# Kernel tuning notes

Measured on AMD Instinct MI355X. Metric: run time of the kernel, lower is better.

## Reference

```python
import jax, jax.numpy as jnp
import numpy as np

D_MODEL = 1024
N_HEAD = 16
D_FF = 4096
SEQ = 2048
BATCH = 4
EPS = 1e-5


def setup_inputs() -> dict:
    key = jax.random.key(0)
    ks = jax.random.split(key, 10)
    s = 0.02
    return {
        "src": jax.random.normal(ks[0], (SEQ, BATCH, D_MODEL), jnp.float32),
        "padding_mask": jnp.zeros((BATCH, SEQ), jnp.bool_),
        "w_qkv": jax.random.normal(ks[1], (3 * D_MODEL, D_MODEL), jnp.float32) * s,
        "fc_w": jax.random.normal(ks[2], (D_MODEL, D_MODEL), jnp.float32) * s,
        "fc_b": jnp.zeros((D_MODEL,), jnp.float32),
        "w1": jax.random.normal(ks[3], (D_FF, D_MODEL), jnp.float32) * s,
        "b1": jnp.zeros((D_FF,), jnp.float32),
        "w2": jax.random.normal(ks[4], (D_MODEL, D_FF), jnp.float32) * s,
        "b2": jnp.zeros((D_MODEL,), jnp.float32),
        "g1": jnp.ones((D_MODEL,), jnp.float32),
        "be1": jnp.zeros((D_MODEL,), jnp.float32),
        "g2": jnp.ones((D_MODEL,), jnp.float32),
        "be2": jnp.zeros((D_MODEL,), jnp.float32),
    }


def _layer_norm(x, g, b):
    mu = jnp.mean(x, axis=-1, keepdims=True)
    var = jnp.mean(jnp.square(x - mu), axis=-1, keepdims=True)
    return (x - mu) * jax.lax.rsqrt(var + EPS) * g + b


def _mha(src, padding_mask, w_qkv, fc_w, fc_b):
    L, B, D = src.shape
    H = N_HEAD
    dh = D // H
    qkv = jnp.einsum("lbd,ed->lbe", src, w_qkv)  # (L,B,3D)
    q, k, v = jnp.split(qkv, 3, axis=-1)
    # (L, B*H, dh) -> (B*H, L, dh)
    q = q.reshape(L, B * H, dh).transpose(1, 0, 2)
    k = k.reshape(L, B * H, dh).transpose(1, 0, 2)
    v = v.reshape(L, B * H, dh).transpose(1, 0, 2)
    scores = jnp.einsum("nqd,nkd->nqk", q, k) / np.sqrt(dh).astype(np.float32)
    scores = scores.reshape(B, H, L, L)
    scores = jnp.where(padding_mask[:, None, None, :], -jnp.inf, scores)
    attn = jax.nn.softmax(scores, axis=-1).reshape(B * H, L, L)
    out = jnp.einsum("nqk,nkd->nqd", attn, v)  # (B*H, L, dh)
    out = out.transpose(1, 0, 2).reshape(L, B, D)
    return out @ fc_w.T + fc_b


def reference(src, padding_mask, w_qkv, fc_w, fc_b, w1, b1, w2, b2, g1, be1, g2, be2):
    src2 = _mha(src, padding_mask, w_qkv, fc_w, fc_b)
    src = _layer_norm(src + src2, g1, be1)
    h = jax.nn.relu(src @ w1.T + b1)
    src2 = h @ w2.T + b2
    return _layer_norm(src + src2, g2, be2)
```

## Files before the change

### kernel.cpp

```cpp
#include <hip/hip_runtime.h>
#include <cstdint>
#include <cstddef>

typedef __attribute__((ext_vector_type(8))) short bf16x8;
typedef __attribute__((ext_vector_type(4))) float f32x4;
typedef __attribute__((ext_vector_type(16))) float f32x16;

static __device__ __forceinline__ unsigned short f2bf(float f) {
    union { float f; unsigned u; } v; v.f = f;
    unsigned r = v.u + 0x7FFFu + ((v.u >> 16) & 1u);
    return (unsigned short)(r >> 16);
}
static __device__ __forceinline__ float bf2f(unsigned short u) {
    union { unsigned u; float f; } v; v.u = ((unsigned)u) << 16; return v.f;
}

static __device__ __forceinline__ void gld_lds16(const void* g, void* l) {
    unsigned loff = (unsigned)(size_t)l;
    loff = (unsigned)__builtin_amdgcn_readfirstlane((int)loff);
    __builtin_amdgcn_global_load_lds(
        (const __attribute__((address_space(1))) unsigned int*)(size_t)g,
        (__attribute__((address_space(3))) unsigned int*)(size_t)loff,
        16, 0, 0);
}

__global__ __launch_bounds__(256) void k_cvt5(
    const float* __restrict__ p0, const float* __restrict__ p1,
    const float* __restrict__ p2, const float* __restrict__ p3,
    const float* __restrict__ p4,
    unsigned short* __restrict__ q0, unsigned short* __restrict__ q1,
    unsigned short* __restrict__ q2, unsigned short* __restrict__ q3,
    unsigned short* __restrict__ q4)
{
    const int blk = blockIdx.x;
    const float* in; unsigned short* out; int base;
    if      (blk < 3072)  { in = p0; out = q0; base = blk; }
    else if (blk < 4096)  { in = p1; out = q1; base = blk - 3072; }
    else if (blk < 8192)  { in = p2; out = q2; base = blk - 4096; }
    else if (blk < 12288) { in = p3; out = q3; base = blk - 8192; }
    else                  { in = p4; out = q4; base = blk - 12288; }
    const int i = (base * 256 + threadIdx.x) * 4;
    float4 v = *reinterpret_cast<const float4*>(in + i);
    ushort4 o;
    o.x = f2bf(v.x); o.y = f2bf(v.y); o.z = f2bf(v.z); o.w = f2bf(v.w);
    *reinterpret_cast<ushort4*>(out + i) = o;
}

template<int BM, int MF>
__global__ __launch_bounds__(512, 2) void k_gemm8(
    const unsigned short* __restrict__ A, const unsigned short* __restrict__ W,
    float* __restrict__ Cf, unsigned short* __restrict__ Cb,
    const float* __restrict__ bias,
    int M, int N, int K, int scale_cols, float scale, int relu)
{
    __shared__ unsigned short As[2][BM * 64];
    __shared__ unsigned short Bs[2][256 * 64];
    const int tid = threadIdx.x, wid = tid >> 6, lane = tid & 63;
    const int lr = lane & 15, g16 = (lane >> 4) * 16;
    const int wm = wid >> 2, wn = wid & 3;

    const int nbx = N >> 8;
    const int nwg = gridDim.x;
    const int raw = blockIdx.x;
    const int swz = (raw & 7) * (nwg >> 3) + (raw >> 3);
    const int bm = (swz / nbx) * BM, bn = (swz % nbx) * 256;

    const int rin = tid >> 3;
    const int cole = (((tid & 7) * 16) ^ ((rin & 7) << 4)) >> 1;

    auto STAGE = [&](int bb, int kt1) {
        #pragma unroll
        for (int c = 0; c < BM / 64; ++c)
            gld_lds16(A + (size_t)(bm + c * 64 + rin) * K + kt1 + cole,
                      (char*)As[bb] + c * 8192 + wid * 1024);
        #pragma unroll
        for (int c = 0; c < 4; ++c)
            gld_lds16(W + (size_t)(bn + c * 64 + rin) * K + kt1 + cole,
                      (char*)Bs[bb] + c * 8192 + wid * 1024);
    };

    f32x4 acc[MF][4] = {};

    STAGE(0, 0);
    STAGE(1, 64);
    int cur = 0;

    for (int kt = 0; kt < K; kt += 64) {
        if (kt + 64 < K) {
            if constexpr (BM == 256) asm volatile("s_waitcnt vmcnt(8)" ::: "memory");
            else                     asm volatile("s_waitcnt vmcnt(6)" ::: "memory");
        } else {
            asm volatile("s_waitcnt vmcnt(0)" ::: "memory");
        }
        __builtin_amdgcn_s_barrier();

        const char* Ab = (const char*)As[cur];
        const char* Bb = (const char*)Bs[cur];
        bf16x8 bfr[4][2];

        #pragma unroll
        for (int p = 0; p < MF / 2; ++p) {
            bf16x8 af[2][2];
            #pragma unroll
            for (int mi = 0; mi < 2; ++mi)
                #pragma unroll
                for (int kk = 0; kk < 2; ++kk) {
                    const int row = wm * (MF * 16) + (2 * p + mi) * 16 + lr;
                    af[mi][kk] = *reinterpret_cast<const bf16x8*>(
                        Ab + row * 128 + ((kk * 64 + g16) ^ ((row & 7) << 4)));
                }
            if (p == 0) {
                #pragma unroll
                for (int n = 0; n < 4; ++n)
                    #pragma unroll
                    for (int kk = 0; kk < 2; ++kk) {
                        const int row = wn * 64 + n * 16 + lr;
                        bfr[n][kk] = *reinterpret_cast<const bf16x8*>(
                            Bb + row * 128 + ((kk * 64 + g16) ^ ((row & 7) << 4)));
                    }
            }
            __builtin_amdgcn_s_barrier();
            __builtin_amdgcn_s_setprio(1);
            #pragma unroll
            for (int mi = 0; mi < 2; ++mi)
                #pragma unroll
                for (int n = 0; n < 4; ++n)
                    #pragma unroll
                    for (int kk = 0; kk < 2; ++kk)
                        acc[2 * p + mi][n] = __builtin_amdgcn_mfma_f32_16x16x32_bf16(
                            af[mi][kk], bfr[n][kk], acc[2 * p + mi][n], 0, 0, 0);
            __builtin_amdgcn_s_setprio(0);
            __builtin_amdgcn_s_barrier();
        }
        if (kt + 128 < K) STAGE(cur, kt + 128);
        cur ^= 1;
    }

    #pragma unroll
    for (int m = 0; m < MF; ++m) {
        #pragma unroll
        for (int n = 0; n < 4; ++n) {
            const int col = bn + wn * 64 + n * 16 + lr;
            const float bv = bias ? bias[col] : 0.0f;
            const float sc = (col < scale_cols) ? scale : 1.0f;
            #pragma unroll
            for (int r = 0; r < 4; ++r) {
                const int row = bm + wm * (MF * 16) + m * 16 + (lane >> 4) * 4 + r;
                float v = acc[m][n][r] * sc + bv;
                if (relu) v = fmaxf(v, 0.0f);
                if (Cb) Cb[(size_t)row * N + col] = f2bf(v);
                else    Cf[(size_t)row * N + col] = v;
            }
        }
    }
}

__global__ __launch_bounds__(256) void k_vtrans(
    const unsigned short* __restrict__ qkv, unsigned short* __restrict__ vt)
{
    __shared__ unsigned short T[64][72];
    const int n = blockIdx.y, b = n >> 4, h = n & 15;
    const int l0 = blockIdx.x * 64;
    const int tid = threadIdx.x;
    {
        const int l = tid >> 2, d = (tid & 3) * 16;
        const unsigned short* p = qkv + (size_t)(l0 + l) * 12288 + b * 3072 + 2048 + h * 64 + d;
        *reinterpret_cast<bf16x8*>(&T[l][d])     = *reinterpret_cast<const bf16x8*>(p);
        *reinterpret_cast<bf16x8*>(&T[l][d + 8]) = *reinterpret_cast<const bf16x8*>(p + 8);
    }
    __syncthreads();
    {
        const int d = tid >> 2, lc = (tid & 3) * 16;
        unsigned short tmp[16];
        #pragma unroll
        for (int j = 0; j < 16; ++j) tmp[j] = T[lc + j][d];
        unsigned short* q = vt + ((size_t)n * 64 + d) * 2048 + l0 + lc;
        *reinterpret_cast<bf16x8*>(q)     = *reinterpret_cast<bf16x8*>(tmp);
        *reinterpret_cast<bf16x8*>(q + 8) = *reinterpret_cast<bf16x8*>(tmp + 8);
    }
}

__global__ __launch_bounds__(512) void k_attn(
    const unsigned short* __restrict__ qkv,
    const unsigned short* __restrict__ vt,
    const unsigned char* __restrict__ mask,
    unsigned short* __restrict__ out)
{
    __shared__ unsigned short Ks[2][64 * 64];
    __shared__ unsigned short Vs[2][64 * 64];
    const int tid = threadIdx.x, wid = tid >> 6, lane = tid & 63;
    const int q32 = lane & 31, hi = lane >> 5;
    const int raw = blockIdx.x;
    const int swz = (raw & 7) * 64 + (raw >> 3);
    const int n = swz >> 3, qblk = swz & 7;
    const int b = n >> 4, h = n & 15;
    const int qbase = qblk * 256 + wid * 32;
    const size_t SL = 12288;

    bf16x8 qf[4];
    {
        const unsigned short* qrow = qkv + (size_t)(qbase + q32) * SL + (size_t)b * 3072 + h * 64;
        #pragma unroll
        for (int t = 0; t < 4; ++t)
            qf[t] = *reinterpret_cast<const bf16x8*>(qrow + t * 16 + hi * 8);
    }

    bool anym;
    {
        const uint4* mp = reinterpret_cast<const uint4*>(mask + b * 2048);
        uint4 m0 = mp[lane * 2], m1 = mp[lane * 2 + 1];
        unsigned mo = m0.x | m0.y | m0.z | m0.w | m1.x | m1.y | m1.z | m1.w;
        anym = __any(mo != 0);
    }

    const int sw = (q32 & 7) << 4;
    int koff[4], voff[2][2];
    #pragma unroll
    for (int t = 0; t < 4; ++t) koff[t] = q32 * 128 + ((t * 32 + hi * 16) ^ sw);
    #pragma unroll
    for (int ks = 0; ks < 2; ++ks)
        #pragma unroll
        for (int hf = 0; hf < 2; ++hf)
            voff[ks][hf] = q32 * 128 + ((ks * 64 + hf * 32 + hi * 16) ^ sw);

    const int soff = wid * 1024 + lane * 16;
    const int srow = soff >> 7;
    const int sbc  = (soff & 127) ^ ((srow & 7) << 4);
    const unsigned short* kgbase = qkv + (size_t)b * 3072 + 1024 + h * 64;
    const unsigned short* vgbase = vt + (size_t)n * 64 * 2048;

    #define STAGE(buf, kt)                                                            \
        do {                                                                          \
            gld_lds16(kgbase + (size_t)((kt) + srow) * SL + (sbc >> 1),               \
                      (char*)Ks[buf] + wid * 1024);                                   \
            gld_lds16(vgbase + (size_t)srow * 2048 + (kt) + (sbc >> 1),               \
                      (char*)Vs[buf] + wid * 1024);                                   \
        } while (0)

    f32x16 o0 = {}, o1 = {}, o2 = {};
    union { unsigned w[4]; bf16x8 v; } onesf;
    onesf.w[0] = 0x3F803F80u; onesf.w[1] = 0x3F803F80u;
    onesf.w[2] = 0x3F803F80u; onesf.w[3] = 0x3F803F80u;

    STAGE(0, 0);
    int cur = 0;

    for (int kt = 0; kt < 2048; kt += 64) {
        __syncthreads();
        if (kt + 64 < 2048) STAGE(cur ^ 1, kt + 64);
        const char* Kb = (const char*)Ks[cur];
        const char* Vb = (const char*)Vs[cur];

        #pragma unroll
        for (int ks = 0; ks < 2; ++ks) {
            f32x16 s = {};
            __builtin_amdgcn_s_setprio(1);
            #pragma unroll
            for (int t = 0; t < 4; ++t) {
                const bf16x8 kf = *reinterpret_cast<const bf16x8*>(Kb + ks * 4096 + koff[t]);
                s = __builtin_amdgcn_mfma_f32_32x32x16_bf16(kf, qf[t], s, 0, 0, 0);
            }
            __builtin_amdgcn_s_setprio(0);

            if (anym) {
                #pragma unroll
                for (int r = 0; r < 16; ++r) {
                    const int kl = (r & 3) + 8 * (r >> 2) + 4 * hi;
                    if (mask[b * 2048 + kt + ks * 32 + kl]) s[r] = -3e8f;
                }
            }

            #pragma unroll
            for (int i = 0; i < 16; ++i) s[i] = __builtin_amdgcn_exp2f(s[i]);

            unsigned pk[8];
            #pragma unroll
            for (int i = 0; i < 8; ++i)
                asm("v_cvt_pk_bf16_f32 %0, %1, %2" : "=v"(pk[i]) : "v"(s[2 * i]), "v"(s[2 * i + 1]));
            asm("v_permlane32_swap_b32 %0, %1" : "+v"(pk[2]), "+v"(pk[0]));
            asm("v_permlane32_swap_b32 %0, %1" : "+v"(pk[3]), "+v"(pk[1]));
            asm("v_permlane32_swap_b32 %0, %1" : "+v"(pk[6]), "+v"(pk[4]));
            asm("v_permlane32_swap_b32 %0, %1" : "+v"(pk[7]), "+v"(pk[5]));
            union { unsigned w[4]; bf16x8 v; } pb0, pb1;
            pb0.w[0] = pk[0]; pb0.w[1] = pk[1]; pb0.w[2] = pk[2]; pb0.w[3] = pk[3];
            pb1.w[0] = pk[4]; pb1.w[1] = pk[5]; pb1.w[2] = pk[6]; pb1.w[3] = pk[7];

            const bf16x8 v00 = *reinterpret_cast<const bf16x8*>(Vb + voff[ks][0]);
            const bf16x8 v01 = *reinterpret_cast<const bf16x8*>(Vb + voff[ks][1]);
            const bf16x8 v10 = *reinterpret_cast<const bf16x8*>(Vb + 4096 + voff[ks][0]);
            const bf16x8 v11 = *reinterpret_cast<const bf16x8*>(Vb + 4096 + voff[ks][1]);
            __builtin_amdgcn_s_setprio(1);
            o0 = __builtin_amdgcn_mfma_f32_32x32x16_bf16(v00, pb0.v, o0, 0, 0, 0);
            o0 = __builtin_amdgcn_mfma_f32_32x32x16_bf16(v01, pb1.v, o0, 0, 0, 0);
            o1 = __builtin_amdgcn_mfma_f32_32x32x16_bf16(v10, pb0.v, o1, 0, 0, 0);
            o1 = __builtin_amdgcn_mfma_f32_32x32x16_bf16(v11, pb1.v, o1, 0, 0, 0);
            o2 = __builtin_amdgcn_mfma_f32_32x32x16_bf16(onesf.v, pb0.v, o2, 0, 0, 0);
            o2 = __builtin_amdgcn_mfma_f32_32x32x16_bf16(onesf.v, pb1.v, o2, 0, 0, 0);
            __builtin_amdgcn_s_setprio(0);
        }
        cur ^= 1;
    }
    #undef STAGE

    const float rl = 1.0f / o2[0];
    unsigned short* orow = out + ((size_t)(qbase + q32) * 4 + b) * 1024 + h * 64;
    #pragma unroll
    for (int q4 = 0; q4 < 4; ++q4) {
        unsigned w0, w1, w2, w3;
        asm("v_cvt_pk_bf16_f32 %0, %1, %2" : "=v"(w0) : "v"(o0[q4 * 4 + 0] * rl), "v"(o0[q4 * 4 + 1] * rl));
        asm("v_cvt_pk_bf16_f32 %0, %1, %2" : "=v"(w1) : "v"(o0[q4 * 4 + 2] * rl), "v"(o0[q4 * 4 + 3] * rl));
        asm("v_cvt_pk_bf16_f32 %0, %1, %2" : "=v"(w2) : "v"(o1[q4 * 4 + 0] * rl), "v"(o1[q4 * 4 + 1] * rl));
        asm("v_cvt_pk_bf16_f32 %0, %1, %2" : "=v"(w3) : "v"(o1[q4 * 4 + 2] * rl), "v"(o1[q4 * 4 + 3] * rl));
        uint2 ua; ua.x = w0; ua.y = w1;
        uint2 ub; ub.x = w2; ub.y = w3;
        *reinterpret_cast<uint2*>(orow + q4 * 8 + hi * 4)      = ua;
        *reinterpret_cast<uint2*>(orow + 32 + q4 * 8 + hi * 4) = ub;
    }
}

template<int OUTF>
__global__ __launch_bounds__(256) void k_add_ln(
    const unsigned short* __restrict__ x, const unsigned short* __restrict__ y,
    const float* __restrict__ gamma, const float* __restrict__ beta,
    float* __restrict__ outf, unsigned short* __restrict__ outb)
{
    const int row = blockIdx.x * 4 + (threadIdx.x >> 6);
    const int lane = threadIdx.x & 63;
    const size_t base = (size_t)row * 1024;
    float v[16];
    float s = 0.0f, ss = 0.0f;
    #pragma unroll
    for (int i = 0; i < 4; ++i) {
        const int c = lane * 4 + i * 256;
        ushort4 a = *reinterpret_cast<const ushort4*>(x + base + c);
        ushort4 d = *reinterpret_cast<const ushort4*>(y + base + c);
        v[i * 4 + 0] = bf2f(a.x) + bf2f(d.x); v[i * 4 + 1] = bf2f(a.y) + bf2f(d.y);
        v[i * 4 + 2] = bf2f(a.z) + bf2f(d.z); v[i * 4 + 3] = bf2f(a.w) + bf2f(d.w);
        #pragma unroll
        for (int j = 0; j < 4; ++j) { s += v[i * 4 + j]; ss += v[i * 4 + j] * v[i * 4 + j]; }
    }
    #pragma unroll
    for (int o = 1; o < 64; o <<= 1) { s += __shfl_xor(s, o); ss += __shfl_xor(ss, o); }
    const float mu = s * (1.0f / 1024.0f);
    const float var = ss * (1.0f / 1024.0f) - mu * mu;
    const float rstd = rsqrtf(var + 1e-5f);
    #pragma unroll
    for (int i = 0; i < 4; ++i) {
        const int c = lane * 4 + i * 256;
        float4 gq = *reinterpret_cast<const float4*>(gamma + c);
        float4 bq = *reinterpret_cast<const float4*>(beta + c);
        float o0 = (v[i * 4 + 0] - mu) * rstd * gq.x + bq.x;
        float o1 = (v[i * 4 + 1] - mu) * rstd * gq.y + bq.y;
        float o2 = (v[i * 4 + 2] - mu) * rstd * gq.z + bq.z;
        float o3 = (v[i * 4 + 3] - mu) * rstd * gq.w + bq.w;
        if (OUTF) {
            float4 o; o.x = o0; o.y = o1; o.z = o2; o.w = o3;
            *reinterpret_cast<float4*>(outf + base + c) = o;
        } else {
            ushort4 ob;
            ob.x = f2bf(o0); ob.y = f2bf(o1); ob.z = f2bf(o2); ob.w = f2bf(o3);
            *reinterpret_cast<ushort4*>(outb + base + c) = ob;
        }
    }
}

extern "C" void kernel_launch(void* const* d_in, const int* in_sizes, int n_in,
                              void* d_out, int out_size, void* d_ws, size_t ws_size,
                              hipStream_t stream) {
    const float* src  = (const float*)d_in[0];
    const unsigned char* mask = (const unsigned char*)d_in[1];
    const float* w_qkv = (const float*)d_in[2];
    const float* fc_w = (const float*)d_in[3];
    const float* fc_b = (const float*)d_in[4];
    const float* w1   = (const float*)d_in[5];
    const float* b1   = (const float*)d_in[6];
    const float* w2   = (const float*)d_in[7];
    const float* b2   = (const float*)d_in[8];
    const float* g1   = (const float*)d_in[9];
    const float* be1  = (const float*)d_in[10];
    const float* g2   = (const float*)d_in[11];
    const float* be2  = (const float*)d_in[12];
    float* out = (float*)d_out;

    char* ws = (char*)d_ws;
    size_t o = 0;
    auto take = [&](size_t nbytes) { size_t p = o; o += (nbytes + 255) & ~(size_t)255; return p; };
    unsigned short* wqkv_b = (unsigned short*)(ws + take((size_t)3072 * 1024 * 2));
    unsigned short* fcw_b  = (unsigned short*)(ws + take((size_t)1024 * 1024 * 2));
    unsigned short* w1_b   = (unsigned short*)(ws + take((size_t)4096 * 1024 * 2));
    unsigned short* w2_b   = (unsigned short*)(ws + take((size_t)1024 * 4096 * 2));
    unsigned short* src_b  = (unsigned short*)(ws + take((size_t)8192 * 1024 * 2));
    unsigned short* qkv_b  = (unsigned short*)(ws + take((size_t)8192 * 3072 * 2));
    unsigned short* attn_b = (unsigned short*)(ws + take((size_t)8192 * 1024 * 2));
    unsigned short* h_b    = (unsigned short*)(ws + take((size_t)8192 * 4096 * 2));
    unsigned short* proj_b = qkv_b;
    unsigned short* y_b    = qkv_b;
    unsigned short* x1_b   = src_b;
    unsigned short* vt_b   = h_b;

    k_cvt5<<<dim3(20480), 256, 0, stream>>>(w_qkv, fc_w, w1, w2, src,
                                            wqkv_b, fcw_b, w1_b, w2_b, src_b);

    k_gemm8<256, 8><<<dim3((8192 / 256) * (3072 / 256)), 512, 0, stream>>>(
        src_b, wqkv_b, nullptr, qkv_b, nullptr, 8192, 3072, 1024, 1024, 0.18033688011112042f, 0);

    k_vtrans<<<dim3(32, 64), 256, 0, stream>>>(qkv_b, vt_b);

    k_attn<<<dim3(512), 512, 0, stream>>>(qkv_b, vt_b, mask, attn_b);

    k_gemm8<128, 4><<<dim3((8192 / 128) * (1024 / 256)), 512, 0, stream>>>(
        attn_b, fcw_b, nullptr, proj_b, fc_b, 8192, 1024, 1024, 0, 1.0f, 0);

    k_add_ln<0><<<dim3(8192 / 4), 256, 0, stream>>>(src_b, proj_b, g1, be1, nullptr, x1_b);

    k_gemm8<256, 8><<<dim3((8192 / 256) * (4096 / 256)), 512, 0, stream>>>(
        x1_b, w1_b, nullptr, h_b, b1, 8192, 4096, 1024, 0, 1.0f, 1);

    k_gemm8<128, 4><<<dim3((8192 / 128) * (1024 / 256)), 512, 0, stream>>>(
        h_b, w2_b, nullptr, y_b, b2, 8192, 1024, 4096, 0, 1.0f, 0);

    k_add_ln<1><<<dim3(8192 / 4), 256, 0, stream>>>(x1_b, y_b, g2, be2, out, nullptr);
}
```

Before: 408.3 us.

## Process two 32-row query tiles per wave in attention to reuse K/V fragments

Each attention wave now computes 64 query rows as two 32-row tiles that share every K and V fragment read from LDS, doubling MFMA work per LDS load. Blocks cover 512 queries and the grid is halved to 256 blocks. This reduces LDS read traffic and staging overhead per unit of compute, and gives two independent MFMA chains to interleave. The cost is doubled accumulator registers and fewer waves in flight across the GPU, which may hurt latency hiding or cause spills.

```diff
diff --git a/kernel.cpp b/kernel.cpp
--- a/kernel.cpp
+++ b/kernel.cpp
@@ -191,18 +191,21 @@
     const int tid = threadIdx.x, wid = tid >> 6, lane = tid & 63;
     const int q32 = lane & 31, hi = lane >> 5;
     const int raw = blockIdx.x;
-    const int swz = (raw & 7) * 64 + (raw >> 3);
-    const int n = swz >> 3, qblk = swz & 7;
+    const int swz = (raw & 7) * 32 + (raw >> 3);
+    const int n = swz >> 2, qblk = swz & 3;
     const int b = n >> 4, h = n & 15;
-    const int qbase = qblk * 256 + wid * 32;
+    const int qbase = qblk * 512 + wid * 64;
     const size_t SL = 12288;
 
-    bf16x8 qf[4];
+    bf16x8 qfa[4], qfb[4];
     {
-        const unsigned short* qrow = qkv + (size_t)(qbase + q32) * SL + (size_t)b * 3072 + h * 64;
-        #pragma unroll
-        for (int t = 0; t < 4; ++t)
-            qf[t] = *reinterpret_cast<const bf16x8*>(qrow + t * 16 + hi * 8);
+        const unsigned short* qra = qkv + (size_t)(qbase + q32) * SL + (size_t)b * 3072 + h * 64;
+        const unsigned short* qrb = qra + 32 * SL;
+        #pragma unroll
+        for (int t = 0; t < 4; ++t) {
+            qfa[t] = *reinterpret_cast<const bf16x8*>(qra + t * 16 + hi * 8);
+            qfb[t] = *reinterpret_cast<const bf16x8*>(qrb + t * 16 + hi * 8);
+        }
     }
 
     bool anym;
@@ -237,7 +240,8 @@
                       (char*)Vs[buf] + wid * 1024);                                   \
         } while (0)
 
-    f32x16 o0 = {}, o1 = {}, o2 = {};
+    f32x16 o0a = {}, o1a = {}, o2a = {};
+    f32x16 o0b = {}, o1b = {}, o2b = {};
     union { unsigned w[4]; bf16x8 v; } onesf;
     onesf.w[0] = 0x3F803F80u; onesf.w[1] = 0x3F803F80u;
     onesf.w[2] = 0x3F803F80u; onesf.w[3] = 0x3F803F80u;
@@ -253,68 +257,101 @@
 
         #pragma unroll
         for (int ks = 0; ks < 2; ++ks) {
-            f32x16 s = {};
+            bf16x8 kf0 = *reinterpret_cast<const bf16x8*>(Kb + ks * 4096 + koff[0]);
+            bf16x8 kf1 = *reinterpret_cast<const bf16x8*>(Kb + ks * 4096 + koff[1]);
+            bf16x8 kf2 = *reinterpret_cast<const bf16x8*>(Kb + ks * 4096 + koff[2]);
+            bf16x8 kf3 = *reinterpret_cast<const bf16x8*>(Kb + ks * 4096 + koff[3]);
+            f32x16 sa = {}, sb = {};
             __builtin_amdgcn_s_setprio(1);
-            #pragma unroll
-            for (int t = 0; t < 4; ++t) {
-                const bf16x8 kf = *reinterpret_cast<const bf16x8*>(Kb + ks * 4096 + koff[t]);
-                s = __builtin_amdgcn_mfma_f32_32x32x16_bf16(kf, qf[t], s, 0, 0, 0);
-            }
+            sa = __builtin_amdgcn_mfma_f32_32x32x16_bf16(kf0, qfa[0], sa, 0, 0, 0);
+            sb = __builtin_amdgcn_mfma_f32_32x32x16_bf16(kf0, qfb[0], sb, 0, 0, 0);
+            sa = __builtin_amdgcn_mfma_f32_32x32x16_bf16(kf1, qfa[1], sa, 0, 0, 0);
+            sb = __builtin_amdgcn_mfma_f32_32x32x16_bf16(kf1, qfb[1], sb, 0, 0, 0);
+            sa = __builtin_amdgcn_mfma_f32_32x32x16_bf16(kf2, qfa[2], sa, 0, 0, 0);
+            sb = __builtin_amdgcn_mfma_f32_32x32x16_bf16(kf2, qfb[2], sb, 0, 0, 0);
+            sa = __builtin_amdgcn_mfma_f32_32x32x16_bf16(kf3, qfa[3], sa, 0, 0, 0);
+            sb = __builtin_amdgcn_mfma_f32_32x32x16_bf16(kf3, qfb[3], sb, 0, 0, 0);
             __builtin_amdgcn_s_setprio(0);
 
             if (anym) {
                 #pragma unroll
                 for (int r = 0; r < 16; ++r) {
                     const int kl = (r & 3) + 8 * (r >> 2) + 4 * hi;
-                    if (mask[b * 2048 + kt + ks * 32 + kl]) s[r] = -3e8f;
+                    if (mask[b * 2048 + kt + ks * 32 + kl]) { sa[r] = -3e8f; sb[r] = -3e8f; }
                 }
             }
 
             #pragma unroll
-            for (int i = 0; i < 16; ++i) s[i] = __builtin_amdgcn_exp2f(s[i]);
-
-            unsigned pk[8];
-            #pragma unroll
-            for (int i = 0; i < 8; ++i)
-                asm("v_cvt_pk_bf16_f32 %0, %1, %2" : "=v"(pk[i]) : "v"(s[2 * i]), "v"(s[2 * i + 1]));
-            asm("v_permlane32_swap_b32 %0, %1" : "+v"(pk[2]), "+v"(pk[0]));
-            asm("v_permlane32_swap_b32 %0, %1" : "+v"(pk[3]), "+v"(pk[1]));
-            asm("v_permlane32_swap_b32 %0, %1" : "+v"(pk[6]), "+v"(pk[4]));
-            asm("v_permlane32_swap_b32 %0, %1" : "+v"(pk[7]), "+v"(pk[5]));
-            union { unsigned w[4]; bf16x8 v; } pb0, pb1;
-            pb0.w[0] = pk[0]; pb0.w[1] = pk[1]; pb0.w[2] = pk[2]; pb0.w[3] = pk[3];
-            pb1.w[0] = pk[4]; pb1.w[1] = pk[5]; pb1.w[2] = pk[6]; pb1.w[3] = pk[7];
+            for (int i = 0; i < 16; ++i) sa[i] = __builtin_amdgcn_exp2f(sa[i]);
+            #pragma unroll
+            for (int i = 0; i < 16; ++i) sb[i] = __builtin_amdgcn_exp2f(sb[i]);
+
+            unsigned pka[8], pkb[8];
+            #pragma unroll
+            for (int i = 0; i < 8; ++i) {
+                asm("v_cvt_pk_bf16_f32 %0, %1, %2" : "=v"(pka[i]) : "v"(sa[2 * i]), "v"(sa[2 * i + 1]));
+                asm("v_cvt_pk_bf16_f32 %0, %1, %2" : "=v"(pkb[i]) : "v"(sb[2 * i]), "v"(sb[2 * i + 1]));
+            }
+            asm("v_permlane32_swap_b32 %0, %1" : "+v"(pka[2]), "+v"(pka[0]));
+            asm("v_permlane32_swap_b32 %0, %1" : "+v"(pka[3]), "+v"(pka[1]));
+            asm("v_permlane32_swap_b32 %0, %1" : "+v"(pka[6]), "+v"(pka[4]));
+            asm("v_permlane32_swap_b32 %0, %1" : "+v"(pka[7]), "+v"(pka[5]));
+            asm("v_permlane32_swap_b32 %0, %1" : "+v"(pkb[2]), "+v"(pkb[0]));
+            asm("v_permlane32_swap_b32 %0, %1" : "+v"(pkb[3]), "+v"(pkb[1]));
+            asm("v_permlane32_swap_b32 %0, %1" : "+v"(pkb[6]), "+v"(pkb[4]));
+            asm("v_permlane32_swap_b32 %0, %1" : "+v"(pkb[7]), "+v"(pkb[5]));
+            union { unsigned w[4]; bf16x8 v; } pa0, pa1, pb0, pb1;
+            pa0.w[0] = pka[0]; pa0.w[1] = pka[1]; pa0.w[2] = pka[2]; pa0.w[3] = pka[3];
+            pa1.w[0] = pka[4]; pa1.w[1] = pka[5]; pa1.w[2] = pka[6]; pa1.w[3] = pka[7];
+            pb0.w[0] = pkb[0]; pb0.w[1] = pkb[1]; pb0.w[2] = pkb[2]; pb0.w[3] = pkb[3];
+            pb1.w[0] = pkb[4]; pb1.w[1] = pkb[5]; pb1.w[2] = pkb[6]; pb1.w[3] = pkb[7];
 
             const bf16x8 v00 = *reinterpret_cast<const bf16x8*>(Vb + voff[ks][0]);
             const bf16x8 v01 = *reinterpret_cast<const bf16x8*>(Vb + voff[ks][1]);
             const bf16x8 v10 = *reinterpret_cast<const bf16x8*>(Vb + 4096 + voff[ks][0]);
             const bf16x8 v11 = *reinterpret_cast<const bf16x8*>(Vb + 4096 + voff[ks][1]);
             __builtin_amdgcn_s_setprio(1);
-            o0 = __builtin_amdgcn_mfma_f32_32x32x16_bf16(v00, pb0.v, o0, 0, 0, 0);
-            o0 = __builtin_amdgcn_mfma_f32_32x32x16_bf16(v01, pb1.v, o0, 0, 0, 0);
-            o1 = __builtin_amdgcn_mfma_f32_32x32x16_bf16(v10, pb0.v, o1, 0, 0, 0);
-            o1 = __builtin_amdgcn_mfma_f32_32x32x16_bf16(v11, pb1.v, o1, 0, 0, 0);
-            o2 = __builtin_amdgcn_mfma_f32_32x32x16_bf16(onesf.v, pb0.v, o2, 0, 0, 0);
-            o2 = __builtin_amdgcn_mfma_f32_32x32x16_bf16(onesf.v, pb1.v, o2, 0, 0, 0);
+            o0a = __builtin_amdgcn_mfma_f32_32x32x16_bf16(v00, pa0.v, o0a, 0, 0, 0);
+            o0b = __builtin_amdgcn_mfma_f32_32x32x16_bf16(v00, pb0.v, o0b, 0, 0, 0);
+            o0a = __builtin_amdgcn_mfma_f32_32x32x16_bf16(v01, pa1.v, o0a, 0, 0, 0);
+            o0b = __builtin_amdgcn_mfma_f32_32x32x16_bf16(v01, pb1.v, o0b, 0, 0, 0);
+            o1a = __builtin_amdgcn_mfma_f32_32x32x16_bf16(v10, pa0.v, o1a, 0, 0, 0);
+            o1b = __builtin_amdgcn_mfma_f32_32x32x16_bf16(v10, pb0.v, o1b, 0, 0, 0);
+            o1a = __builtin_amdgcn_mfma_f32_32x32x16_bf16(v11, pa1.v, o1a, 0, 0, 0);
+            o1b = __builtin_amdgcn_mfma_f32_32x32x16_bf16(v11, pb1.v, o1b, 0, 0, 0);
+            o2a = __builtin_amdgcn_mfma_f32_32x32x16_bf16(onesf.v, pa0.v, o2a, 0, 0, 0);
+            o2b = __builtin_amdgcn_mfma_f32_32x32x16_bf16(onesf.v, pb0.v, o2b, 0, 0, 0);
+            o2a = __builtin_amdgcn_mfma_f32_32x32x16_bf16(onesf.v, pa1.v, o2a, 0, 0, 0);
+            o2b = __builtin_amdgcn_mfma_f32_32x32x16_bf16(onesf.v, pb1.v, o2b, 0, 0, 0);
             __builtin_amdgcn_s_setprio(0);
         }
         cur ^= 1;
     }
     #undef STAGE
 
-    const float rl = 1.0f / o2[0];
-    unsigned short* orow = out + ((size_t)(qbase + q32) * 4 + b) * 1024 + h * 64;
+    const float rla = 1.0f / o2a[0];
+    const float rlb = 1.0f / o2b[0];
+    unsigned short* orowa = out + ((size_t)(qbase + q32) * 4 + b) * 1024 + h * 64;
+    unsigned short* orowb = orowa + (size_t)32 * 4096;
     #pragma unroll
     for (int q4 = 0; q4 < 4; ++q4) {
         unsigned w0, w1, w2, w3;
-        asm("v_cvt_pk_bf16_f32 %0, %1, %2" : "=v"(w0) : "v"(o0[q4 * 4 + 0] * rl), "v"(o0[q4 * 4 + 1] * rl));
-        asm("v_cvt_pk_bf16_f32 %0, %1, %2" : "=v"(w1) : "v"(o0[q4 * 4 + 2] * rl), "v"(o0[q4 * 4 + 3] * rl));
-        asm("v_cvt_pk_bf16_f32 %0, %1, %2" : "=v"(w2) : "v"(o1[q4 * 4 + 0] * rl), "v"(o1[q4 * 4 + 1] * rl));
-        asm("v_cvt_pk_bf16_f32 %0, %1, %2" : "=v"(w3) : "v"(o1[q4 * 4 + 2] * rl), "v"(o1[q4 * 4 + 3] * rl));
+        asm("v_cvt_pk_bf16_f32 %0, %1, %2" : "=v"(w0) : "v"(o0a[q4 * 4 + 0] * rla), "v"(o0a[q4 * 4 + 1] * rla));
+        asm("v_cvt_pk_bf16_f32 %0, %1, %2" : "=v"(w1) : "v"(o0a[q4 * 4 + 2] * rla), "v"(o0a[q4 * 4 + 3] * rla));
+        asm("v_cvt_pk_bf16_f32 %0, %1, %2" : "=v"(w2) : "v"(o1a[q4 * 4 + 0] * rla), "v"(o1a[q4 * 4 + 1] * rla));
+        asm("v_cvt_pk_bf16_f32 %0, %1, %2" : "=v"(w3) : "v"(o1a[q4 * 4 + 2] * rla), "v"(o1a[q4 * 4 + 3] * rla));
         uint2 ua; ua.x = w0; ua.y = w1;
         uint2 ub; ub.x = w2; ub.y = w3;
-        *reinterpret_cast<uint2*>(orow + q4 * 8 + hi * 4)      = ua;
-        *reinterpret_cast<uint2*>(orow + 32 + q4 * 8 + hi * 4) = ub;
+        *reinterpret_cast<uint2*>(orowa + q4 * 8 + hi * 4)      = ua;
+        *reinterpret_cast<uint2*>(orowa + 32 + q4 * 8 + hi * 4) = ub;
+        asm("v_cvt_pk_bf16_f32 %0, %1, %2" : "=v"(w0) : "v"(o0b[q4 * 4 + 0] * rlb), "v"(o0b[q4 * 4 + 1] * rlb));
+        asm("v_cvt_pk_bf16_f32 %0, %1, %2" : "=v"(w1) : "v"(o0b[q4 * 4 + 2] * rlb), "v"(o0b[q4 * 4 + 3] * rlb));
+        asm("v_cvt_pk_bf16_f32 %0, %1, %2" : "=v"(w2) : "v"(o1b[q4 * 4 + 0] * rlb), "v"(o1b[q4 * 4 + 1] * rlb));
+        asm("v_cvt_pk_bf16_f32 %0, %1, %2" : "=v"(w3) : "v"(o1b[q4 * 4 + 2] * rlb), "v"(o1b[q4 * 4 + 3] * rlb));
+        uint2 uc; uc.x = w0; uc.y = w1;
+        uint2 ud; ud.x = w2; ud.y = w3;
+        *reinterpret_cast<uint2*>(orowb + q4 * 8 + hi * 4)      = uc;
+        *reinterpret_cast<uint2*>(orowb + 32 + q4 * 8 + hi * 4) = ud;
     }
 }
 
@@ -406,7 +443,7 @@
 
     k_vtrans<<<dim3(32, 64), 256, 0, stream>>>(qkv_b, vt_b);
 
-    k_attn<<<dim3(512), 512, 0, stream>>>(qkv_b, vt_b, mask, attn_b);
+    k_attn<<<dim3(256), 512, 0, stream>>>(qkv_b, vt_b, mask, attn_b);
 
     k_gemm8<128, 4><<<dim3((8192 / 128) * (1024 / 256)), 512, 0, stream>>>(
         attn_b, fcw_b, nullptr, proj_b, fc_b, 8192, 1024, 1024, 0, 1.0f, 0);
```

After: 394.2 us. 1.04x faster.
